# Kernel tuning notes

Measured on AMD Instinct MI355X. Metric: run time of the kernel, lower is better.

## Reference

```python
import jax, jax.numpy as jnp
import numpy as np

L = 64          # lattice side
NSITES = L * L  # 4096
HALF = NSITES // 2
B = 16384
H = 128         # hidden width of s/t MLPs
SLOPE = 0.2     # tf.nn.leaky_relu default alpha

# checkerboard parity indices (static, evenodd = 0)
_coords = np.arange(NSITES)
_parity = (_coords // L + _coords % L) % 2
IDX_A = jnp.asarray(np.where(_parity == 0)[0], dtype=jnp.int32)  # [HALF]
IDX_B = jnp.asarray(np.where(_parity == 1)[0], dtype=jnp.int32)  # [HALF]


def setup_inputs() -> dict:
    key = jax.random.key(0)
    ks = jax.random.split(key, 8)
    scale = 0.05  # small init keeps exp(-s) well-behaved
    return {
        "z":    jax.random.normal(ks[0], (B, NSITES), dtype=jnp.float32),
        "s_W0": jax.random.normal(ks[1], (HALF, H), dtype=jnp.float32) * scale,
        "s_W1": jax.random.normal(ks[2], (H, H), dtype=jnp.float32) * scale,
        "s_W2": jax.random.normal(ks[3], (H, HALF), dtype=jnp.float32) * scale,
        "s_b2": jnp.zeros((HALF,), dtype=jnp.float32),
        "t_W0": jax.random.normal(ks[4], (HALF, H), dtype=jnp.float32) * scale,
        "t_W1": jax.random.normal(ks[5], (H, H), dtype=jnp.float32) * scale,
        "t_W2": jax.random.normal(ks[6], (H, HALF), dtype=jnp.float32) * scale,
        "t_b2": jnp.zeros((HALF,), dtype=jnp.float32),
    }


def _mlp(x, W0, W1, W2, b2):
    # Dense(no bias)+leaky_relu x2, then Dense(with bias), matching the keras stack
    h = jax.nn.leaky_relu(x @ W0, negative_slope=SLOPE)
    h = jax.nn.leaky_relu(h @ W1, negative_slope=SLOPE)
    return h @ W2 + b2


def reference(z, s_W0, s_W1, s_W2, s_b2, t_W0, t_W1, t_W2, t_b2):
    z_a = z[:, IDX_A]                       # [B, HALF] gather (even sites)
    z_b = z[:, IDX_B]                       # [B, HALF] gather (odd sites)
    s_out = _mlp(z_a, s_W0, s_W1, s_W2, s_b2)   # [B, HALF]
    t_a = _mlp(z_a, t_W0, t_W1, t_W2, t_b2)     # [B, HALF]
    s_a = jnp.exp(-s_out)
    f_b = (z_b - t_a) * s_a                 # affine coupling
    # scatter back (disjoint indices -> set is equivalent to scatter_nd add)
    f = jnp.zeros_like(z).at[:, IDX_A].set(z_a).at[:, IDX_B].set(f_b)
    d = jnp.sum(s_out, axis=1)              # logdetjacfwd: sum of s(z_a)
    return (f, d)
```

## Files before the change

### kernel.cpp

```cpp
#include <hip/hip_runtime.h>
#include <hip/hip_bf16.h>

#define BATCH  16384
#define SLOPE  0.2f
#define BM     32

typedef __attribute__((ext_vector_type(8))) short bf16x8;
typedef __attribute__((ext_vector_type(4))) float f32x4;
typedef __attribute__((ext_vector_type(4))) float fx4;
typedef __attribute__((ext_vector_type(2))) float fx2;

#define OFF_SW0T 0
#define OFF_TW0T 262144
#define OFF_SW1T 524288
#define OFF_TW1T 540672
#define OFF_SW2T 557056
#define OFF_TW2T 819200

__device__ __forceinline__ unsigned short f2bf(float f) {
    unsigned int u = __float_as_uint(f);
    u += 0x7FFFu + ((u >> 16) & 1u);
    return (unsigned short)(u >> 16);
}

__global__ void conv_w(const float* __restrict__ sW0, const float* __restrict__ sW1,
                       const float* __restrict__ sW2, const float* __restrict__ tW0,
                       const float* __restrict__ tW1, const float* __restrict__ tW2,
                       unsigned short* __restrict__ ws) {
    const int total = 262144 + 16384 + 262144;
    for (int i = blockIdx.x * blockDim.x + threadIdx.x; i < total;
         i += gridDim.x * blockDim.x) {
        if (i < 262144) {
            int k = i >> 7, n = i & 127;
            int ks = (k & ~63) | ((((k >> 3) & 7) ^ (n & 7)) << 3) | (k & 7);
            ws[OFF_SW0T + n * 2048 + ks] = f2bf(sW0[i]);
            ws[OFF_TW0T + n * 2048 + ks] = f2bf(tW0[i]);
        } else if (i < 262144 + 16384) {
            int j = i - 262144;
            int k = j >> 7, n = j & 127;
            ws[OFF_SW1T + n * 128 + k] = f2bf(sW1[j]);
            ws[OFF_TW1T + n * 128 + k] = f2bf(tW1[j]);
        } else {
            int j = i - (262144 + 16384);
            int k = j >> 11, n = j & 2047;
            int ks = ((((k >> 3) & 15) ^ (n & 7)) << 3) | (k & 7);
            ws[OFF_SW2T + n * 128 + ks] = f2bf(sW2[j]);
            ws[OFF_TW2T + n * 128 + ks] = f2bf(tW2[j]);
        }
    }
}

__global__ __launch_bounds__(256, 2) void coupling_main(
    const float* __restrict__ z,
    const float* __restrict__ s_b2,
    const float* __restrict__ t_b2,
    const unsigned short* __restrict__ ws,
    float* __restrict__ f_out,
    float* __restrict__ d_vec) {

    __shared__ __align__(16) unsigned char LDSbuf[73728];
    unsigned short* HA = (unsigned short*)(LDSbuf + 8192);
    unsigned short* HB = (unsigned short*)(LDSbuf + 24576);
    float* Dred = (float*)(LDSbuf + 65536);

    const int tid  = threadIdx.x;
    const int wave = tid >> 6;
    const int lane = tid & 63;
    const int l15  = lane & 15;
    const int l4   = lane >> 4;
    const int brow = blockIdx.x * BM;

    const char* wsb = (const char*)ws;
    const fx4* __restrict__ zf4 = (const fx4*)z;
    const fx2* __restrict__ zf2 = (const fx2*)z;
    fx2* __restrict__ ff2 = (fx2*)f_out;

    auto ldzTo = [&](fx4 (&zr)[4], int c) {
        #pragma unroll
        for (int q = 0; q < 4; ++q) {
            const int f = tid + 256 * q;
            const int row = f >> 5, col16 = f & 31;
            zr[q] = __builtin_nontemporal_load(
                zf4 + (size_t)(brow + row) * 1024 + c * 32 + col16);
        }
    };
    auto wrzFrom = [&](fx4 (&zr)[4], int b) {
        #pragma unroll
        for (int q = 0; q < 4; ++q) {
            const int f = tid + 256 * q;
            const int row = f >> 5, col16 = f & 31;
            const int par = (col16 >> 4) & 1;
            const float a0 = par ? zr[q].y : zr[q].x;
            const float a1 = par ? zr[q].w : zr[q].z;
            const unsigned int pk = (unsigned int)f2bf(a0) | ((unsigned int)f2bf(a1) << 16);
            *(unsigned int*)(LDSbuf + b * 4096 + row * 128 +
                             (((col16 >> 2) ^ (row & 7)) << 4) + (col16 & 3) * 4) = pk;
        }
    };
    auto stageW0 = [&](int b, int c) {
        #pragma unroll
        for (int jj = 0; jj < 8; ++jj) {
            const char* g = wsb + (size_t)(wave * 64 + jj * 8 + (lane >> 3)) * 4096
                            + c * 128 + (lane & 7) * 16;
            void* l = LDSbuf + 8192 + b * 32768 + (wave * 64 + jj * 8) * 128;
            __builtin_amdgcn_global_load_lds(
                (const __attribute__((address_space(1))) unsigned int*)g,
                (__attribute__((address_space(3))) unsigned int*)l, 16, 0, 0);
        }
    };

    f32x4 acc0[2][4] = {};
    auto cmp0 = [&](int cb) {
        const char* Az = (const char*)(LDSbuf + cb * 4096);
        const char* Wt = (const char*)(LDSbuf + 8192 + cb * 32768);
        bf16x8 af[2][2], wf[4][2];
        #pragma unroll
        for (int m = 0; m < 2; ++m)
            #pragma unroll
            for (int k2 = 0; k2 < 2; ++k2) {
                const int row = m * 16 + l15;
                af[m][k2] = *(const bf16x8*)(Az + row * 128 +
                              ((k2 * 64 + l4 * 16) ^ ((row & 7) << 4)));
            }
        #pragma unroll
        for (int n2 = 0; n2 < 4; ++n2)
            #pragma unroll
            for (int k2 = 0; k2 < 2; ++k2) {
                const int g = wave * 64 + n2 * 16 + l15;
                wf[n2][k2] = *(const bf16x8*)(Wt + g * 128 +
                               ((k2 * 64 + l4 * 16) ^ ((g & 7) << 4)));
            }
        #pragma unroll
        for (int n2 = 0; n2 < 4; ++n2)
            #pragma unroll
            for (int k2 = 0; k2 < 2; ++k2)
                #pragma unroll
                for (int m = 0; m < 2; ++m)
                    acc0[m][n2] = __builtin_amdgcn_mfma_f32_16x16x32_bf16(
                        af[m][k2], wf[n2][k2], acc0[m][n2], 0, 0, 0);
    };

    fx4 zA[4], zB[4];
    auto phase = [&](int p, int cb, fx4 (&zLd)[4], fx4 (&zWr)[4]) {
        if (p + 1 < 32) stageW0(cb ^ 1, p + 1);
        if (p + 2 < 32) ldzTo(zLd, p + 2);
        cmp0(cb);
        if (p + 1 < 32) wrzFrom(zWr, cb ^ 1);
        if (p + 2 < 32)
            asm volatile("s_waitcnt lgkmcnt(0) vmcnt(4)" ::: "memory");
        else
            asm volatile("s_waitcnt lgkmcnt(0) vmcnt(0)" ::: "memory");
        __builtin_amdgcn_s_barrier();
        __builtin_amdgcn_sched_barrier(0);
    };

    ldzTo(zB, 0);
    stageW0(0, 0);
    wrzFrom(zB, 0);
    ldzTo(zB, 1);
    asm volatile("s_waitcnt lgkmcnt(0) vmcnt(4)" ::: "memory");
    __builtin_amdgcn_s_barrier();
    __builtin_amdgcn_sched_barrier(0);

    #pragma unroll 1
    for (int gIt = 0; gIt < 16; ++gIt) {
        phase(2 * gIt,     0, zA, zB);
        phase(2 * gIt + 1, 1, zB, zA);
    }

    #pragma unroll
    for (int m = 0; m < 2; ++m)
        #pragma unroll
        for (int n2 = 0; n2 < 4; ++n2)
            #pragma unroll
            for (int r = 0; r < 4; ++r) {
                float v = acc0[m][n2][r];
                v = v > 0.0f ? v : SLOPE * v;
                const int row = m * 16 + l4 * 4 + r;
                const int col = wave * 64 + n2 * 16 + l15;
                HA[row * 256 + (col ^ ((row & 7) << 3))] = f2bf(v);
            }
    __syncthreads();

    f32x4 acc1[2][4] = {};
    const int net1 = wave >> 1;
    #pragma unroll
    for (int k4 = 0; k4 < 4; ++k4) {
        bf16x8 ahv[2];
        #pragma unroll
        for (int m = 0; m < 2; ++m) {
            const int row = m * 16 + l15;
            ahv[m] = *(const bf16x8*)&HA[row * 256 +
                       ((net1 * 128 + k4 * 32 + l4 * 8) ^ ((row & 7) << 3))];
        }
        #pragma unroll
        for (int n2 = 0; n2 < 4; ++n2) {
            const bf16x8 w = *(const bf16x8*)&ws[OFF_SW1T +
                (size_t)(wave * 64 + n2 * 16 + l15) * 128 + k4 * 32 + l4 * 8];
            #pragma unroll
            for (int m = 0; m < 2; ++m)
                acc1[m][n2] = __builtin_amdgcn_mfma_f32_16x16x32_bf16(
                    ahv[m], w, acc1[m][n2], 0, 0, 0);
        }
    }
    __syncthreads();
    #pragma unroll
    for (int m = 0; m < 2; ++m)
        #pragma unroll
        for (int n2 = 0; n2 < 4; ++n2)
            #pragma unroll
            for (int r = 0; r < 4; ++r) {
                float v = acc1[m][n2][r];
                v = v > 0.0f ? v : SLOPE * v;
                const int row = m * 16 + l4 * 4 + r;
                const int col = wave * 64 + n2 * 16 + l15;
                HB[row * 256 + (col ^ ((row & 7) << 3))] = f2bf(v);
            }
    __syncthreads();

    const int par = wave >> 1;

    bf16x8 ahs[2][4], aht[2][4];
    #pragma unroll
    for (int m = 0; m < 2; ++m)
        #pragma unroll
        for (int k4 = 0; k4 < 4; ++k4) {
            const int row = m * 16 + l15;
            const int kc = k4 * 32 + l4 * 8;
            ahs[m][k4] = *(const bf16x8*)&HB[row * 256 + (kc ^ ((row & 7) << 3))];
            aht[m][k4] = *(const bf16x8*)&HB[row * 256 + ((128 + kc) ^ ((row & 7) << 3))];
        }
    __syncthreads();

    auto stageW2 = [&](int b, int c2) {
        #pragma unroll
        for (int jj = 0; jj < 8; ++jj) {
            const int r  = wave * 32 + jj * 4 + (lane >> 4);
            const int pr = c2 * 64 + (r & 63);
            const char* g = wsb + (size_t)((r >> 6) ? OFF_TW2T : OFF_SW2T) * 2
                            + (size_t)pr * 256 + (lane & 15) * 16;
            void* l = LDSbuf + b * 32768 + (wave * 32 + jj * 4) * 256;
            __builtin_amdgcn_global_load_lds(
                (const __attribute__((address_space(1))) unsigned int*)g,
                (__attribute__((address_space(3))) unsigned int*)l, 16, 0, 0);
        }
    };

    stageW2(0, 0);
    __syncthreads();

    float dsum[2][4] = {};
    #pragma unroll 1
    for (int c2 = 0; c2 < 32; ++c2) {
        const int cb = c2 & 1;
        if (c2 < 31) stageW2(cb ^ 1, c2 + 1);

        const int j = c2 * 64 + wave * 16 + l15;
        const float sb = s_b2[j];
        const float tb = t_b2[j];
        fx2 zv[2][4];
        #pragma unroll
        for (int m = 0; m < 2; ++m)
            #pragma unroll
            for (int r = 0; r < 4; ++r)
                zv[m][r] = __builtin_nontemporal_load(
                    &zf2[(size_t)(brow + m * 16 + l4 * 4 + r) * 2048 + j]);

        bf16x8 wfs[4], wft[4];
        #pragma unroll
        for (int k4 = 0; k4 < 4; ++k4) {
            const int rs = wave * 16 + l15;
            const int rt = 64 + wave * 16 + l15;
            const int kc = k4 * 64 + l4 * 16;
            wfs[k4] = *(const bf16x8*)(LDSbuf + cb * 32768 + rs * 256 + (kc ^ ((rs & 7) << 4)));
            wft[k4] = *(const bf16x8*)(LDSbuf + cb * 32768 + rt * 256 + (kc ^ ((rt & 7) << 4)));
        }

        f32x4 acc2[2][2] = {};
        #pragma unroll
        for (int k4 = 0; k4 < 4; ++k4)
            #pragma unroll
            for (int m = 0; m < 2; ++m) {
                acc2[0][m] = __builtin_amdgcn_mfma_f32_16x16x32_bf16(
                    ahs[m][k4], wfs[k4], acc2[0][m], 0, 0, 0);
                acc2[1][m] = __builtin_amdgcn_mfma_f32_16x16x32_bf16(
                    aht[m][k4], wft[k4], acc2[1][m], 0, 0, 0);
            }

        #pragma unroll
        for (int m = 0; m < 2; ++m)
            #pragma unroll
            for (int r = 0; r < 4; ++r) {
                const float sv = acc2[0][m][r] + sb;
                const float tv = acc2[1][m][r] + tb;
                const fx2 zp = zv[m][r];
                const float za = par ? zp.y : zp.x;
                const float zb = par ? zp.x : zp.y;
                const float fb = (zb - tv) * __expf(-sv);
                fx2 fv;
                if (par) { fv.x = fb; fv.y = za; }
                else     { fv.x = za; fv.y = fb; }
                __builtin_nontemporal_store(fv,
                    &ff2[(size_t)(brow + m * 16 + l4 * 4 + r) * 2048 + j]);
                dsum[m][r] += sv;
            }
        __syncthreads();
    }

    #pragma unroll
    for (int m = 0; m < 2; ++m)
        #pragma unroll
        for (int r = 0; r < 4; ++r) {
            float v = dsum[m][r];
            v += __shfl_xor(v, 1);
            v += __shfl_xor(v, 2);
            v += __shfl_xor(v, 4);
            v += __shfl_xor(v, 8);
            if (l15 == 0) Dred[wave * 32 + m * 16 + l4 * 4 + r] = v;
        }
    __syncthreads();
    if (tid < BM)
        d_vec[brow + tid] = Dred[tid] + Dred[32 + tid] + Dred[64 + tid] + Dred[96 + tid];
}

extern "C" void kernel_launch(void* const* d_in, const int* in_sizes, int n_in,
                              void* d_out, int out_size, void* d_ws, size_t ws_size,
                              hipStream_t stream) {
    const float* z   = (const float*)d_in[0];
    const float* sW0 = (const float*)d_in[1];
    const float* sW1 = (const float*)d_in[2];
    const float* sW2 = (const float*)d_in[3];
    const float* sb2 = (const float*)d_in[4];
    const float* tW0 = (const float*)d_in[5];
    const float* tW1 = (const float*)d_in[6];
    const float* tW2 = (const float*)d_in[7];
    const float* tb2 = (const float*)d_in[8];

    float* fout = (float*)d_out;
    float* dvec = fout + (size_t)BATCH * 4096;
    unsigned short* ws = (unsigned short*)d_ws;

    hipLaunchKernelGGL(conv_w, dim3(512), dim3(256), 0, stream,
                       sW0, sW1, sW2, tW0, tW1, tW2, ws);
    hipLaunchKernelGGL(coupling_main, dim3(BATCH / BM), dim3(256), 0, stream,
                       z, sb2, tb2, ws, fout, dvec);
}
```

Measured before the change: 183.5 us.

## Software-pipeline epilogue z loads and raise wave priority around MFMA blocks

The final layer loop is unrolled by two with double-buffered register sets so the z values and biases for the next chunk are prefetched while the current chunk's MFMAs and epilogue run. __syncthreads is replaced by explicit s_waitcnt with a partial vmcnt and s_barrier, so in-flight loads are not fully drained each iteration. s_setprio is also raised around the MFMA blocks in all three layers to favour matrix issue. The hand-set vmcnt(18) must match the real number of outstanding loads, and the extra buffers raise register pressure.

New measurement: 193.5 us. 1.05x slower.

```diff
diff --git a/kernel.cpp b/kernel.cpp
--- a/kernel.cpp
+++ b/kernel.cpp
@@ -130,6 +130,7 @@
                 wf[n2][k2] = *(const bf16x8*)(Wt + g * 128 +
                                ((k2 * 64 + l4 * 16) ^ ((g & 7) << 4)));
             }
+        __builtin_amdgcn_s_setprio(1);
         #pragma unroll
         for (int n2 = 0; n2 < 4; ++n2)
             #pragma unroll
@@ -138,6 +139,7 @@
                 for (int m = 0; m < 2; ++m)
                     acc0[m][n2] = __builtin_amdgcn_mfma_f32_16x16x32_bf16(
                         af[m][k2], wf[n2][k2], acc0[m][n2], 0, 0, 0);
+        __builtin_amdgcn_s_setprio(0);
     };
 
     fx4 zA[4], zB[4];
@@ -193,6 +195,7 @@
             ahv[m] = *(const bf16x8*)&HA[row * 256 +
                        ((net1 * 128 + k4 * 32 + l4 * 8) ^ ((row & 7) << 3))];
         }
+        __builtin_amdgcn_s_setprio(1);
         #pragma unroll
         for (int n2 = 0; n2 < 4; ++n2) {
             const bf16x8 w = *(const bf16x8*)&ws[OFF_SW1T +
@@ -202,6 +205,7 @@
                 acc1[m][n2] = __builtin_amdgcn_mfma_f32_16x16x32_bf16(
                     ahv[m], w, acc1[m][n2], 0, 0, 0);
         }
+        __builtin_amdgcn_s_setprio(0);
     }
     __syncthreads();
     #pragma unroll
@@ -246,26 +250,23 @@
         }
     };
 
-    stageW2(0, 0);
-    __syncthreads();
-
     float dsum[2][4] = {};
-    #pragma unroll 1
-    for (int c2 = 0; c2 < 32; ++c2) {
-        const int cb = c2 & 1;
-        if (c2 < 31) stageW2(cb ^ 1, c2 + 1);
-
+
+    fx2 zvA[2][4], zvB[2][4];
+    float sbA, tbA, sbB, tbB;
+    auto ldzEp = [&](fx2 (&zv)[2][4], float& sb, float& tb, int c2) {
         const int j = c2 * 64 + wave * 16 + l15;
-        const float sb = s_b2[j];
-        const float tb = t_b2[j];
-        fx2 zv[2][4];
+        sb = s_b2[j];
+        tb = t_b2[j];
         #pragma unroll
         for (int m = 0; m < 2; ++m)
             #pragma unroll
             for (int r = 0; r < 4; ++r)
                 zv[m][r] = __builtin_nontemporal_load(
                     &zf2[(size_t)(brow + m * 16 + l4 * 4 + r) * 2048 + j]);
-
+    };
+
+    auto l2body = [&](fx2 (&zv)[2][4], float sb, float tb, int c2, int cb) {
         bf16x8 wfs[4], wft[4];
         #pragma unroll
         for (int k4 = 0; k4 < 4; ++k4) {
@@ -275,8 +276,8 @@
             wfs[k4] = *(const bf16x8*)(LDSbuf + cb * 32768 + rs * 256 + (kc ^ ((rs & 7) << 4)));
             wft[k4] = *(const bf16x8*)(LDSbuf + cb * 32768 + rt * 256 + (kc ^ ((rt & 7) << 4)));
         }
-
         f32x4 acc2[2][2] = {};
+        __builtin_amdgcn_s_setprio(1);
         #pragma unroll
         for (int k4 = 0; k4 < 4; ++k4)
             #pragma unroll
@@ -286,7 +287,8 @@
                 acc2[1][m] = __builtin_amdgcn_mfma_f32_16x16x32_bf16(
                     aht[m][k4], wft[k4], acc2[1][m], 0, 0, 0);
             }
-
+        __builtin_amdgcn_s_setprio(0);
+        const int j = c2 * 64 + wave * 16 + l15;
         #pragma unroll
         for (int m = 0; m < 2; ++m)
             #pragma unroll
@@ -304,7 +306,39 @@
                     &ff2[(size_t)(brow + m * 16 + l4 * 4 + r) * 2048 + j]);
                 dsum[m][r] += sv;
             }
-        __syncthreads();
+    };
+
+    stageW2(0, 0);
+    ldzEp(zvA, sbA, tbA, 0);
+    __syncthreads();
+
+    #pragma unroll 1
+    for (int it = 0; it < 16; ++it) {
+        {
+            const int c2 = 2 * it;
+            stageW2(1, c2 + 1);
+            __builtin_amdgcn_sched_barrier(0);
+            ldzEp(zvB, sbB, tbB, c2 + 1);
+            l2body(zvA, sbA, tbA, c2, 0);
+            asm volatile("s_waitcnt lgkmcnt(0) vmcnt(18)" ::: "memory");
+            __builtin_amdgcn_s_barrier();
+            __builtin_amdgcn_sched_barrier(0);
+        }
+        {
+            const int c2 = 2 * it + 1;
+            if (c2 < 31) {
+                stageW2(0, c2 + 1);
+                __builtin_amdgcn_sched_barrier(0);
+                ldzEp(zvA, sbA, tbA, c2 + 1);
+            }
+            l2body(zvB, sbB, tbB, c2, 1);
+            if (c2 < 31)
+                asm volatile("s_waitcnt lgkmcnt(0) vmcnt(18)" ::: "memory");
+            else
+                asm volatile("s_waitcnt lgkmcnt(0) vmcnt(0)" ::: "memory");
+            __builtin_amdgcn_s_barrier();
+            __builtin_amdgcn_sched_barrier(0);
+        }
     }
 
     #pragma unroll
```
